# Optimization experiments

Measured on AMD Instinct MI355X. Metric: run time of the kernel, lower is better.

The kernel has to match this reference:

```python
import jax, jax.numpy as jnp
import numpy as np

D = 64          # hidden_dim
H = 4           # num_attention_heads
L = 3           # num_layers
NUM_SEG = 32    # graphs per batch
N_MOL, N_PROT = 4096, 8192
E_MOL, E_PROT = 65536, 262144
LN_EPS = 1e-5


def linear(x, w, b):
    return x @ w + b


def gine_conv(x, edge_index, edge_attr, w1, b1, w2, b2, num_nodes):
    # GINEConv (eps=0): nn(x_i + sum_{j->i} relu(x_j + e_ij))
    src, dst = edge_index[0], edge_index[1]
    msg = jax.nn.relu(x[src] + edge_attr)                      # [E, D]
    agg = jax.ops.segment_sum(msg, dst, num_segments=num_nodes)
    h = jax.nn.relu(linear(x + agg, w1, b1))
    return linear(h, w2, b2)


def cross_attn(q_nodes, k_nodes, qkv_w, qkv_b):
    # qkv_w: [3, D, D] stacked (Q, K, V)
    dh = D // H
    Q = (q_nodes @ qkv_w[0] + qkv_b[0]).reshape(-1, H, dh)
    K = (k_nodes @ qkv_w[1] + qkv_b[1]).reshape(-1, H, dh)
    V = (k_nodes @ qkv_w[2] + qkv_b[2]).reshape(-1, H, dh)
    scale = jnp.asarray(dh, Q.dtype) ** 0.5
    scores = jnp.einsum('qhd,khd->hqk', Q, K) / scale          # [H, Nq, Nk]
    attn = jax.nn.softmax(scores, axis=-1)
    out = jnp.einsum('hqk,khd->qhd', attn, V)                  # [Nq, H, dh]
    return out.reshape(q_nodes.shape[0], D)


def layer_norm(x, g, b):
    mu = x.mean(-1, keepdims=True)
    var = x.var(-1, keepdims=True)
    return (x - mu) / jnp.sqrt(var + LN_EPS) * g + b


def mean_pool(x, batch):
    s = jax.ops.segment_sum(x, batch, num_segments=NUM_SEG)
    c = jax.ops.segment_sum(jnp.ones((x.shape[0],), x.dtype), batch, num_segments=NUM_SEG)
    return s / jnp.maximum(c, 1.0)[:, None]


def setup_inputs() -> dict:
    key = jax.random.key(0)
    ks = iter(jax.random.split(key, 64))
    s = 0.05
    inp = {}
    inp['mol_x'] = jax.random.normal(next(ks), (N_MOL, 11), jnp.float32)
    inp['prot_x'] = jax.random.normal(next(ks), (N_PROT, 15), jnp.float32)
    inp['mol_edge_attr'] = jax.random.normal(next(ks), (E_MOL, 10), jnp.float32)
    inp['prot_edge_attr'] = jax.random.normal(next(ks), (E_PROT, 10), jnp.float32)
    inp['init_node_mol_w'] = jax.random.normal(next(ks), (11, D), jnp.float32) * s
    inp['init_node_mol_b'] = jnp.zeros((D,), jnp.float32)
    inp['init_node_prot_w'] = jax.random.normal(next(ks), (15, D), jnp.float32) * s
    inp['init_node_prot_b'] = jnp.zeros((D,), jnp.float32)
    inp['init_edge_mol_w'] = jax.random.normal(next(ks), (10, D), jnp.float32) * s
    inp['init_edge_mol_b'] = jnp.zeros((D,), jnp.float32)
    inp['init_edge_prot_w'] = jax.random.normal(next(ks), (10, D), jnp.float32) * s
    inp['init_edge_prot_b'] = jnp.zeros((D,), jnp.float32)
    for g in ['mol', 'prot']:
        inp[f'gine_{g}_w1'] = jax.random.normal(next(ks), (L, D, D), jnp.float32) * s
        inp[f'gine_{g}_b1'] = jnp.zeros((L, D), jnp.float32)
        inp[f'gine_{g}_w2'] = jax.random.normal(next(ks), (L, D, D), jnp.float32) * s
        inp[f'gine_{g}_b2'] = jnp.zeros((L, D), jnp.float32)
    inp['m2p_qkv_w'] = jax.random.normal(next(ks), (L, 3, D, D), jnp.float32) * s
    inp['m2p_qkv_b'] = jnp.zeros((L, 3, D), jnp.float32)
    inp['p2m_qkv_w'] = jax.random.normal(next(ks), (L, 3, D, D), jnp.float32) * s
    inp['p2m_qkv_b'] = jnp.zeros((L, 3, D), jnp.float32)
    inp['ln_mol_g'] = jnp.ones((L, D), jnp.float32)
    inp['ln_mol_b'] = jnp.zeros((L, D), jnp.float32)
    inp['ln_prot_g'] = jnp.ones((L, D), jnp.float32)
    inp['ln_prot_b'] = jnp.zeros((L, D), jnp.float32)
    inp['fc1_w'] = jax.random.normal(next(ks), (2 * D, D), jnp.float32) * s
    inp['fc1_b'] = jnp.zeros((D,), jnp.float32)
    inp['fc2_w'] = jax.random.normal(next(ks), (D, 1), jnp.float32) * s
    inp['fc2_b'] = jnp.zeros((1,), jnp.float32)
    inp['mol_edge_index'] = jax.random.randint(next(ks), (2, E_MOL), 0, N_MOL, jnp.int32)
    inp['prot_edge_index'] = jax.random.randint(next(ks), (2, E_PROT), 0, N_PROT, jnp.int32)
    inp['mol_batch'] = jnp.sort(jax.random.randint(next(ks), (N_MOL,), 0, NUM_SEG, jnp.int32))
    inp['prot_batch'] = jnp.sort(jax.random.randint(next(ks), (N_PROT,), 0, NUM_SEG, jnp.int32))
    return inp


def reference(mol_x, prot_x, mol_edge_attr, prot_edge_attr,
              init_node_mol_w, init_node_mol_b, init_node_prot_w, init_node_prot_b,
              init_edge_mol_w, init_edge_mol_b, init_edge_prot_w, init_edge_prot_b,
              gine_mol_w1, gine_mol_b1, gine_mol_w2, gine_mol_b2,
              gine_prot_w1, gine_prot_b1, gine_prot_w2, gine_prot_b2,
              m2p_qkv_w, m2p_qkv_b, p2m_qkv_w, p2m_qkv_b,
              ln_mol_g, ln_mol_b, ln_prot_g, ln_prot_b,
              fc1_w, fc1_b, fc2_w, fc2_b,
              mol_edge_index, prot_edge_index, mol_batch, prot_batch):
    x_mol = linear(mol_x, init_node_mol_w, init_node_mol_b)
    x_prot = linear(prot_x, init_node_prot_w, init_node_prot_b)
    ea_mol = linear(mol_edge_attr, init_edge_mol_w, init_edge_mol_b)
    ea_prot = linear(prot_edge_attr, init_edge_prot_w, init_edge_prot_b)
    n_mol, n_prot = x_mol.shape[0], x_prot.shape[0]
    for l in range(L):
        h_mol = jax.nn.relu(gine_conv(x_mol, mol_edge_index, ea_mol,
                                      gine_mol_w1[l], gine_mol_b1[l],
                                      gine_mol_w2[l], gine_mol_b2[l], n_mol))
        h_prot = jax.nn.relu(gine_conv(x_prot, prot_edge_index, ea_prot,
                                       gine_prot_w1[l], gine_prot_b1[l],
                                       gine_prot_w2[l], gine_prot_b2[l], n_prot))
        a_mol = cross_attn(h_mol, h_prot, m2p_qkv_w[l], m2p_qkv_b[l])
        a_prot = cross_attn(h_prot, h_mol, p2m_qkv_w[l], p2m_qkv_b[l])
        x_mol = layer_norm(h_mol + a_mol, ln_mol_g[l], ln_mol_b[l])
        x_prot = layer_norm(h_prot + a_prot, ln_prot_g[l], ln_prot_b[l])
    z = jnp.concatenate([mean_pool(x_mol, mol_batch), mean_pool(x_prot, prot_batch)], axis=1)
    h = jax.nn.relu(z @ fc1_w + fc1_b)
    out = jax.nn.sigmoid(h @ fc2_w + fc2_b)
    return out.squeeze(-1)   # [NUM_SEG]
```

## Files before the change

### kernel.cpp

```cpp
#include <hip/hip_runtime.h>
#include <cstddef>

typedef _Float16 f16x4 __attribute__((ext_vector_type(4)));
typedef __fp16 h16x2 __attribute__((ext_vector_type(2)));
typedef float f32x4 __attribute__((ext_vector_type(4)));

__device__ __forceinline__ f32x4 mfma16(f16x4 a, f16x4 b, f32x4 c) {
  return __builtin_amdgcn_mfma_f32_16x16x16f16(a, b, c, 0, 0, 0);
}

__device__ __forceinline__ float fast_exp2(float x) {
#if __has_builtin(__builtin_amdgcn_exp2f)
  return __builtin_amdgcn_exp2f(x);
#else
  return exp2f(x);
#endif
}

#define QSCALE (0.25f * 1.44269504f)
#define NSPLIT 8
#define NMC 4096
#define NPC 8192
#define EMC 65536
#define EPC 262144
#define NTOT (NMC + NPC)
#define ETOT (EMC + EPC)

__global__ __launch_bounds__(256) void init_embed_dual(
    const float* __restrict__ inm, const float* __restrict__ Wm,
    const float* __restrict__ bm, float* __restrict__ outm,
    const float* __restrict__ inp, const float* __restrict__ Wp,
    const float* __restrict__ bp, float* __restrict__ outp)
{
  int idx = blockIdx.x * 256 + threadIdx.x;
  const float *in, *W, *bb;
  float* out;
  int Kin;
  if (idx < NMC * 64) {
    in = inm; W = Wm; bb = bm; out = outm; Kin = 11;
  } else {
    idx -= NMC * 64;
    if (idx >= NPC * 64) return;
    in = inp; W = Wp; bb = bp; out = outp; Kin = 15;
  }
  int n = idx >> 6, o = idx & 63;
  float acc = bb[o];
  const float* row = in + (size_t)n * Kin;
  for (int k = 0; k < Kin; k++) acc += row[k] * W[k * 64 + o];
  out[idx] = acc;
}

__global__ __launch_bounds__(256) void deg_hist_kernel(
    const int* __restrict__ eim, const int* __restrict__ eip, int* __restrict__ deg)
{
  int idx = blockIdx.x * 256 + threadIdx.x;
  if (idx >= ETOT) return;
  int dst = (idx < EMC) ? eim[EMC + idx] : (eip[EPC + (idx - EMC)] + NMC);
  atomicAdd(&deg[dst], 1);
}

__global__ __launch_bounds__(1024) void scan_kernel(
    const int* __restrict__ deg, int* __restrict__ rowStart, int* __restrict__ cursor)
{
  __shared__ int part[1024];
  int t = threadIdx.x;
  int base = t * 12;
  int local[12];
  int s = 0;
  #pragma unroll
  for (int i = 0; i < 12; i++) { local[i] = s; s += deg[base + i]; }
  part[t] = s;
  __syncthreads();
  #pragma unroll
  for (int d = 1; d < 1024; d <<= 1) {
    int v = (t >= d) ? part[t - d] : 0;
    __syncthreads();
    part[t] += v;
    __syncthreads();
  }
  int prefix = (t == 0) ? 0 : part[t - 1];
  #pragma unroll
  for (int i = 0; i < 12; i++) {
    int v = prefix + local[i];
    rowStart[base + i] = v;
    cursor[base + i] = v;
  }
  if (t == 1023) rowStart[NTOT] = prefix + s;
}

__global__ __launch_bounds__(256) void fill_kernel(
    const int* __restrict__ eim, const int* __restrict__ eip,
    int* __restrict__ cursor, int* __restrict__ srcPerm, int* __restrict__ slotOf)
{
  int idx = blockIdx.x * 256 + threadIdx.x;
  if (idx >= ETOT) return;
  int src, dst;
  if (idx < EMC) {
    src = eim[idx]; dst = eim[EMC + idx];
  } else {
    int e = idx - EMC; src = eip[e]; dst = eip[EPC + e] + NMC;
  }
  int slot = atomicAdd(&cursor[dst], 1);
  srcPerm[slot] = src;
  slotOf[idx] = slot;
}

__global__ __launch_bounds__(256) void attr_perm_kernel(
    const int* __restrict__ slotOf,
    const float* __restrict__ attrm, const float* __restrict__ attrp,
    float* __restrict__ attrPerm)
{
  int idx = blockIdx.x * 256 + threadIdx.x;
  int e = idx >> 4, k = idx & 15;
  if (e >= ETOT || k >= 12) return;
  float v = 0.f;
  if (k < 10)
    v = (e < EMC) ? attrm[(size_t)e * 10 + k] : attrp[(size_t)(e - EMC) * 10 + k];
  attrPerm[(size_t)slotOf[e] * 12 + k] = v;
}

__global__ __launch_bounds__(256) void ea_lin_kernel(
    const float* __restrict__ attrPerm,
    const float* __restrict__ Wem, const float* __restrict__ bem,
    const float* __restrict__ Wep, const float* __restrict__ bep,
    _Float16* __restrict__ eaPerm)
{
  __shared__ __align__(16) float sAttr[128 * 12];
  __shared__ float sWe[10 * 64];
  __shared__ float sBe[64];
  int t = threadIdx.x;
  int s0 = blockIdx.x * 128;
  const float* We = (s0 < EMC) ? Wem : Wep;
  const float* be = (s0 < EMC) ? bem : bep;
  #pragma unroll
  for (int i = 0; i < 6; i++) {
    int f = t + i * 256;
    sAttr[f] = attrPerm[(size_t)s0 * 12 + f];
  }
  for (int f = t; f < 640; f += 256) sWe[f] = We[f];
  if (t < 64) sBe[t] = be[t];
  __syncthreads();
  int sl = t >> 1;
  int d0 = (t & 1) * 32;
  float at[10];
  #pragma unroll
  for (int k = 0; k < 10; k++) at[k] = sAttr[sl * 12 + k];
  _Float16 outv[32];
  #pragma unroll
  for (int j = 0; j < 32; j++) {
    int d = d0 + j;
    float ea = sBe[d];
    #pragma unroll
    for (int k = 0; k < 10; k++) ea += at[k] * sWe[k * 64 + d];
    outv[j] = (_Float16)ea;
  }
  float4* dst = (float4*)(eaPerm + (size_t)(s0 + sl) * 64 + d0);
  const float4* src = (const float4*)outv;
  #pragma unroll
  for (int j = 0; j < 4; j++) dst[j] = src[j];
}

__global__ __launch_bounds__(256) void gine_gather_kernel(
    const float* __restrict__ xm, const float* __restrict__ xp,
    const int* __restrict__ rowStart, const int* __restrict__ srcPerm,
    const _Float16* __restrict__ eaPerm,
    float* __restrict__ aggm, float* __restrict__ aggp)
{
  int n = (blockIdx.x * 256 + threadIdx.x) >> 6;
  int lane = threadIdx.x & 63;
  if (n >= NTOT) return;
  const float* x;
  float* agg;
  int nl;
  if (n < NMC) { x = xm; agg = aggm; nl = n; }
  else         { x = xp; agg = aggp; nl = n - NMC; }
  int b0 = rowStart[n], b1 = rowStart[n + 1];
  float acc = 0.f;
  int i = b0;
  for (; i + 3 < b1; i += 4) {
    int s0 = srcPerm[i], s1 = srcPerm[i + 1], s2 = srcPerm[i + 2], s3 = srcPerm[i + 3];
    float e0 = (float)eaPerm[(size_t)i * 64 + lane];
    float e1 = (float)eaPerm[(size_t)(i + 1) * 64 + lane];
    float e2 = (float)eaPerm[(size_t)(i + 2) * 64 + lane];
    float e3 = (float)eaPerm[(size_t)(i + 3) * 64 + lane];
    float x0 = x[(size_t)s0 * 64 + lane];
    float x1 = x[(size_t)s1 * 64 + lane];
    float x2 = x[(size_t)s2 * 64 + lane];
    float x3 = x[(size_t)s3 * 64 + lane];
    acc += fmaxf(x0 + e0, 0.f) + fmaxf(x1 + e1, 0.f)
         + fmaxf(x2 + e2, 0.f) + fmaxf(x3 + e3, 0.f);
  }
  for (; i < b1; i++) {
    int src = srcPerm[i];
    float m = x[(size_t)src * 64 + lane] + (float)eaPerm[(size_t)i * 64 + lane];
    acc += fmaxf(m, 0.f);
  }
  agg[(size_t)nl * 64 + lane] = acc;
}

__global__ __launch_bounds__(256) void mlp_proj_dual(
    const float* __restrict__ xm, const float* __restrict__ aggm,
    const float* __restrict__ W1m, const float* __restrict__ B1m,
    const float* __restrict__ W2m, const float* __restrict__ B2m,
    float* __restrict__ hm,
    const float* __restrict__ Wqm, const float* __restrict__ bqm,
    const float* __restrict__ Wkm, const float* __restrict__ bkm,
    const float* __restrict__ Wvm, const float* __restrict__ bvm,
    _Float16* __restrict__ Qom, _Float16* __restrict__ Kom, _Float16* __restrict__ Vtom,
    const float* __restrict__ xp, const float* __restrict__ aggp,
    const float* __restrict__ W1p, const float* __restrict__ B1p,
    const float* __restrict__ W2p, const float* __restrict__ B2p,
    float* __restrict__ hp,
    const float* __restrict__ Wqp, const float* __restrict__ bqp,
    const float* __restrict__ Wkp, const float* __restrict__ bkp,
    const float* __restrict__ Wvp, const float* __restrict__ bvp,
    _Float16* __restrict__ Qop, _Float16* __restrict__ Kop, _Float16* __restrict__ Vtop)
{
  __shared__ __align__(16) float sW[64 * 64];
  __shared__ __align__(16) float sBuf[64 * 68];
  int t = threadIdx.x;
  int b = blockIdx.x;
  const float *x, *agg, *W1, *B1, *W2, *B2, *Wq, *bq, *Wk, *bk, *Wv, *bv;
  float* hg;
  _Float16 *Qo, *Ko, *Vto;
  int n0, N;
  if (b < 64) {
    x = xm; agg = aggm; W1 = W1m; B1 = B1m; W2 = W2m; B2 = B2m; hg = hm;
    Wq = Wqm; bq = bqm; Wk = Wkm; bk = bkm; Wv = Wvm; bv = bvm;
    Qo = Qom; Ko = Kom; Vto = Vtom; n0 = b * 64; N = NMC;
  } else {
    x = xp; agg = aggp; W1 = W1p; B1 = B1p; W2 = W2p; B2 = B2p; hg = hp;
    Wq = Wqp; bq = bqp; Wk = Wkp; bk = bkp; Wv = Wvp; bv = bvp;
    Qo = Qop; Ko = Kop; Vto = Vtop; n0 = (b - 64) * 64; N = NPC;
  }
  int n = t >> 2, kk = t & 3;
  float acc[16];

  #pragma unroll
  for (int i = 0; i < 16; i++) {
    int f = t + i * 256;
    size_t g = (size_t)n0 * 64 + f;
    sBuf[(f >> 6) * 68 + (f & 63)] = x[g] + agg[g];
    sW[f] = W1[f];
  }
  __syncthreads();
  #pragma unroll
  for (int j = 0; j < 16; j++) acc[j] = B1[kk * 16 + j];
  #pragma unroll
  for (int d = 0; d < 64; d++) {
    float xv = sBuf[n * 68 + d];
    const float* wrow = &sW[d * 64 + kk * 16];
    #pragma unroll
    for (int j = 0; j < 16; j++) acc[j] += xv * wrow[j];
  }
  __syncthreads();
  #pragma unroll
  for (int j = 0; j < 16; j++) sBuf[n * 68 + kk * 16 + j] = fmaxf(acc[j], 0.f);
  #pragma unroll
  for (int i = 0; i < 16; i++) { int f = t + i * 256; sW[f] = W2[f]; }
  __syncthreads();
  #pragma unroll
  for (int j = 0; j < 16; j++) acc[j] = B2[kk * 16 + j];
  #pragma unroll
  for (int d = 0; d < 64; d++) {
    float xv = sBuf[n * 68 + d];
    const float* wrow = &sW[d * 64 + kk * 16];
    #pragma unroll
    for (int j = 0; j < 16; j++) acc[j] += xv * wrow[j];
  }
  float* hop = hg + (size_t)(n0 + n) * 64 + kk * 16;
  #pragma unroll
  for (int j = 0; j < 16; j++) {
    acc[j] = fmaxf(acc[j], 0.f);
    hop[j] = acc[j];
  }
  __syncthreads();
  #pragma unroll
  for (int j = 0; j < 16; j++) sBuf[n * 68 + kk * 16 + j] = acc[j];

  const float* Ws[3] = {Wq, Wk, Wv};
  const float* bs[3] = {bq, bk, bv};
  for (int p = 0; p < 3; p++) {
    if (p > 0) __syncthreads();
    #pragma unroll
    for (int i = 0; i < 16; i++) { int f = t + i * 256; sW[f] = Ws[p][f]; }
    __syncthreads();
    #pragma unroll
    for (int j = 0; j < 16; j++) acc[j] = bs[p][kk * 16 + j];
    #pragma unroll
    for (int d = 0; d < 64; d++) {
      float xv = sBuf[n * 68 + d];
      const float* wrow = &sW[d * 64 + kk * 16];
      #pragma unroll
      for (int j = 0; j < 16; j++) acc[j] += xv * wrow[j];
    }
    if (p == 2) {
      #pragma unroll
      for (int j = 0; j < 16; j++)
        Vto[((size_t)kk * 16 + j) * N + (n0 + n)] = (_Float16)acc[j];
    } else {
      float scale = (p == 0) ? QSCALE : 1.0f;
      _Float16 tmp[16];
      #pragma unroll
      for (int j = 0; j < 16; j++) tmp[j] = (_Float16)(acc[j] * scale);
      _Float16* base = (p == 0) ? Qo : Ko;
      float4* dst = (float4*)(base + ((size_t)kk * N + n0 + n) * 16);
      dst[0] = ((float4*)tmp)[0];
      dst[1] = ((float4*)tmp)[1];
    }
  }
}

__global__ __launch_bounds__(256, 4) void attn_split_kernel(
    const _Float16* __restrict__ Qm, const _Float16* __restrict__ Kp,
    const _Float16* __restrict__ Vtp, float* __restrict__ OPm, float* __restrict__ LPm,
    const _Float16* __restrict__ Qp, const _Float16* __restrict__ Km,
    const _Float16* __restrict__ Vtm, float* __restrict__ OPp, float* __restrict__ LPp)
{
  const int bx = blockIdx.x;
  const _Float16 *Q, *K, *Vt;
  float *Opart, *Lpart;
  int Nq, Nk, qb;
  if (bx < 32) { Q = Qm; K = Kp; Vt = Vtp; Opart = OPm; Lpart = LPm; Nq = NMC; Nk = NPC; qb = bx; }
  else         { Q = Qp; K = Km; Vt = Vtm; Opart = OPp; Lpart = LPp; Nq = NPC; Nk = NMC; qb = bx - 32; }
  const int h = blockIdx.y;
  const int split = blockIdx.z;
  const int Ks = Nk / NSPLIT;
  const int q0 = qb * 128;
  const int t = threadIdx.x;
  const int wave = t >> 6, lane = t & 63;
  const int l16 = lane & 15, quad = lane >> 4;

  f16x4 qf[8];
  #pragma unroll
  for (int g = 0; g < 8; g++)
    qf[g] = *(const f16x4*)(Q + ((size_t)h * Nq + q0 + g * 16 + l16) * 16 + quad * 4);
  const _Float16* Kh = K + (size_t)h * Nk * 16;
  const _Float16* Vh = Vt + ((size_t)h * 16 + l16) * Nk;

  f32x4 oacc[8];
  float lacc[8];
  #pragma unroll
  for (int g = 0; g < 8; g++) { oacc[g] = (f32x4){0.f,0.f,0.f,0.f}; lacc[g] = 0.f; }
  const f32x4 zero = {0.f, 0.f, 0.f, 0.f};
  const h16x2 ones2 = {(__fp16)1.f, (__fp16)1.f};

  union PF { f16x4 v4; h16x2 h2[2]; };

  auto process = [&](const f16x4* kf, const f16x4* vf) {
    #pragma unroll
    for (int g = 0; g < 8; g++) {
      f32x4 s[4];
      #pragma unroll
      for (int c = 0; c < 4; c++) s[c] = mfma16(kf[c], qf[g], zero);
      f16x4 pf[4];
      #pragma unroll
      for (int c = 0; c < 4; c++) {
        float p0 = fast_exp2(s[c][0]);
        float p1 = fast_exp2(s[c][1]);
        float p2 = fast_exp2(s[c][2]);
        float p3 = fast_exp2(s[c][3]);
        PF u;
        u.h2[0] = __builtin_amdgcn_cvt_pkrtz(p0, p1);
        u.h2[1] = __builtin_amdgcn_cvt_pkrtz(p2, p3);
        pf[c] = u.v4;
        lacc[g] = __builtin_amdgcn_fdot2(u.h2[0], ones2, lacc[g], false);
        lacc[g] = __builtin_amdgcn_fdot2(u.h2[1], ones2, lacc[g], false);
      }
      #pragma unroll
      for (int c = 0; c < 4; c++) oacc[g] = mfma16(vf[c], pf[c], oacc[g]);
    }
  };

  const int kend = (split + 1) * Ks;
  int kb = split * Ks + wave * 64;
  for (; kb + 256 < kend; kb += 512) {
    f16x4 kfA[4], vfA[4], kfB[4], vfB[4];
    #pragma unroll
    for (int c = 0; c < 4; c++) {
      kfA[c] = *(const f16x4*)(Kh + (size_t)(kb + c * 16 + l16) * 16 + quad * 4);
      vfA[c] = *(const f16x4*)(Vh + kb + c * 16 + quad * 4);
    }
    #pragma unroll
    for (int c = 0; c < 4; c++) {
      kfB[c] = *(const f16x4*)(Kh + (size_t)(kb + 256 + c * 16 + l16) * 16 + quad * 4);
      vfB[c] = *(const f16x4*)(Vh + kb + 256 + c * 16 + quad * 4);
    }
    process(kfA, vfA);
    process(kfB, vfB);
  }
  for (; kb < kend; kb += 256) {
    f16x4 kf[4], vf[4];
    #pragma unroll
    for (int c = 0; c < 4; c++) {
      kf[c] = *(const f16x4*)(Kh + (size_t)(kb + c * 16 + l16) * 16 + quad * 4);
      vf[c] = *(const f16x4*)(Vh + kb + c * 16 + quad * 4);
    }
    process(kf, vf);
  }

  #pragma unroll
  for (int g = 0; g < 8; g++) {
    lacc[g] += __shfl_xor(lacc[g], 16);
    lacc[g] += __shfl_xor(lacc[g], 32);
  }

  __shared__ float sO[4][4][16][17];
  __shared__ float sLw[8][4][16];
  if (quad == 0) {
    #pragma unroll
    for (int g = 0; g < 8; g++) sLw[g][wave][l16] = lacc[g];
  }
  int q = t >> 4, d = t & 15;
  #pragma unroll
  for (int pass = 0; pass < 2; pass++) {
    __syncthreads();
    #pragma unroll
    for (int gg = 0; gg < 4; gg++) {
      int g = pass * 4 + gg;
      #pragma unroll
      for (int r = 0; r < 4; r++) sO[gg][wave][quad * 4 + r][l16] = oacc[g][r];
    }
    __syncthreads();
    #pragma unroll
    for (int gg = 0; gg < 4; gg++) {
      int g = pass * 4 + gg;
      float O = 0.f;
      #pragma unroll
      for (int w = 0; w < 4; w++) O += sO[gg][w][d][q];
      size_t row = (size_t)split * Nq + q0 + g * 16 + q;
      Opart[row * 64 + h * 16 + d] = O;
      if (d == 0) {
        float L = sLw[g][0][q] + sLw[g][1][q] + sLw[g][2][q] + sLw[g][3][q];
        Lpart[row * 4 + h] = L;
      }
    }
  }
}

__global__ __launch_bounds__(256) void ln_combine_dual(
    const float* __restrict__ hm, const float* __restrict__ Om,
    const float* __restrict__ Lm, const float* __restrict__ gm,
    const float* __restrict__ bm, float* __restrict__ outm,
    const float* __restrict__ hp, const float* __restrict__ Op,
    const float* __restrict__ Lp, const float* __restrict__ gp,
    const float* __restrict__ bp, float* __restrict__ outp)
{
  int idx = blockIdx.x * 256 + threadIdx.x;
  const float *hb, *Opart, *Lpart, *g, *bb;
  float* out;
  int N;
  int totalM = NMC * 64;
  if (idx < totalM) {
    hb = hm; Opart = Om; Lpart = Lm; g = gm; bb = bm; out = outm; N = NMC;
  } else {
    idx -= totalM;
    if (idx >= NPC * 64) return;
    hb = hp; Opart = Op; Lpart = Lp; g = gp; bb = bp; out = outp; N = NPC;
  }
  int n = idx >> 6, d = idx & 63, h = d >> 4;
  float O = 0.f, L = 0.f;
  #pragma unroll
  for (int s = 0; s < NSPLIT; s++) {
    size_t row = (size_t)s * N + n;
    O += Opart[row * 64 + d];
    L += Lpart[row * 4 + h];
  }
  float v = hb[idx] + O / L;
  float sm = v;
  #pragma unroll
  for (int o = 1; o < 64; o <<= 1) sm += __shfl_xor(sm, o);
  float mu = sm * 0.015625f;
  float c = v - mu;
  float q = c * c;
  #pragma unroll
  for (int o = 1; o < 64; o <<= 1) q += __shfl_xor(q, o);
  float var = q * 0.015625f;
  out[idx] = c * rsqrtf(var + 1e-5f) * g[d] + bb[d];
}

__global__ __launch_bounds__(256) void pool_run_kernel(
    const float* __restrict__ xm, const int* __restrict__ bm,
    const float* __restrict__ xp, const int* __restrict__ bp,
    float* __restrict__ sums, float* __restrict__ cnt)
{
  int wid = (blockIdx.x * 256 + threadIdx.x) >> 6;
  int lane = threadIdx.x & 63;
  const float* x;
  const int* batch;
  int n0, colOff, cntOff;
  if (wid < 64) {
    x = xm; batch = bm; n0 = wid * 64; colOff = 0; cntOff = 0;
  } else {
    wid -= 64;
    if (wid >= 128) return;
    x = xp; batch = bp; n0 = wid * 64; colOff = 64; cntOff = 32;
  }
  float acc = 0.f;
  int cur = batch[n0];
  int run = 0;
  for (int i = 0; i < 64; i++) {
    int n = n0 + i;
    int s = batch[n];
    if (s != cur) {
      atomicAdd(&sums[cur * 128 + colOff + lane], acc);
      if (lane == 0) atomicAdd(&cnt[cntOff + cur], (float)run);
      acc = 0.f; run = 0; cur = s;
    }
    acc += x[(size_t)n * 64 + lane];
    run++;
  }
  atomicAdd(&sums[cur * 128 + colOff + lane], acc);
  if (lane == 0) atomicAdd(&cnt[cntOff + cur], (float)run);
}

__global__ __launch_bounds__(256) void final_kernel(
    const float* __restrict__ sums, const float* __restrict__ cnt,
    const float* __restrict__ fc1w, const float* __restrict__ fc1b,
    const float* __restrict__ fc2w, const float* __restrict__ fc2b,
    float* __restrict__ out)
{
  __shared__ float z[32 * 128];
  __shared__ float h1[32 * 64];
  int t = threadIdx.x;
  for (int f = t; f < 32 * 128; f += 256) {
    int s = f >> 7, j = f & 127;
    float c = cnt[(j >> 6) * 32 + s];
    z[f] = sums[f] / fmaxf(c, 1.f);
  }
  __syncthreads();
  for (int f = t; f < 32 * 64; f += 256) {
    int s = f >> 6, o = f & 63;
    float acc = fc1b[o];
    for (int j = 0; j < 128; j++) acc += z[s * 128 + j] * fc1w[j * 64 + o];
    h1[f] = fmaxf(acc, 0.f);
  }
  __syncthreads();
  if (t < 32) {
    float acc = fc2b[0];
    for (int o = 0; o < 64; o++) acc += h1[t * 64 + o] * fc2w[o];
    out[t] = 1.f / (1.f + __expf(-acc));
  }
}

extern "C" void kernel_launch(void* const* d_in, const int* in_sizes, int n_in,
                              void* d_out, int out_size, void* d_ws, size_t ws_size,
                              hipStream_t stream)
{
  (void)in_sizes; (void)n_in; (void)out_size; (void)ws_size;
  const float* mol_x          = (const float*)d_in[0];
  const float* prot_x         = (const float*)d_in[1];
  const float* mol_edge_attr  = (const float*)d_in[2];
  const float* prot_edge_attr = (const float*)d_in[3];
  const float* inm_w = (const float*)d_in[4];
  const float* inm_b = (const float*)d_in[5];
  const float* inp_w = (const float*)d_in[6];
  const float* inp_b = (const float*)d_in[7];
  const float* iem_w = (const float*)d_in[8];
  const float* iem_b = (const float*)d_in[9];
  const float* iep_w = (const float*)d_in[10];
  const float* iep_b = (const float*)d_in[11];
  const float* gm_w1 = (const float*)d_in[12];
  const float* gm_b1 = (const float*)d_in[13];
  const float* gm_w2 = (const float*)d_in[14];
  const float* gm_b2 = (const float*)d_in[15];
  const float* gp_w1 = (const float*)d_in[16];
  const float* gp_b1 = (const float*)d_in[17];
  const float* gp_w2 = (const float*)d_in[18];
  const float* gp_b2 = (const float*)d_in[19];
  const float* m2p_w = (const float*)d_in[20];
  const float* m2p_b = (const float*)d_in[21];
  const float* p2m_w = (const float*)d_in[22];
  const float* p2m_b = (const float*)d_in[23];
  const float* lnm_g = (const float*)d_in[24];
  const float* lnm_b = (const float*)d_in[25];
  const float* lnp_g = (const float*)d_in[26];
  const float* lnp_b = (const float*)d_in[27];
  const float* fc1_w = (const float*)d_in[28];
  const float* fc1_b = (const float*)d_in[29];
  const float* fc2_w = (const float*)d_in[30];
  const float* fc2_b = (const float*)d_in[31];
  const int* mol_ei     = (const int*)d_in[32];
  const int* prot_ei    = (const int*)d_in[33];
  const int* mol_batch  = (const int*)d_in[34];
  const int* prot_batch = (const int*)d_in[35];

  const int NM = NMC, NP = NPC;

  float* ws = (float*)d_ws;
  size_t off = 0;
  auto nxt  = [&](size_t n) { float* p = ws + off; off += n; return p; };
  auto nxtH = [&](size_t n) { _Float16* p = (_Float16*)(ws + off); off += (n + 1) / 2; return p; };
  auto nxtI = [&](size_t n) { int* p = (int*)(ws + off); off += n; return p; };
  float* x_mol    = nxt((size_t)NM * 64);
  float* x_prot   = nxt((size_t)NP * 64);
  float* agg_mol  = nxt((size_t)NM * 64);
  float* agg_prot = nxt((size_t)NP * 64);
  float* h_mol    = nxt((size_t)NM * 64);
  float* h_prot   = nxt((size_t)NP * 64);
  _Float16* Qm  = nxtH((size_t)NM * 64);
  _Float16* Km  = nxtH((size_t)NM * 64);
  _Float16* Vtm = nxtH((size_t)NM * 64);
  _Float16* Qp  = nxtH((size_t)NP * 64);
  _Float16* Kp  = nxtH((size_t)NP * 64);
  _Float16* Vtp = nxtH((size_t)NP * 64);
  float* OPm = nxt((size_t)NSPLIT * NM * 64);
  float* LPm = nxt((size_t)NSPLIT * NM * 4);
  float* OPp = nxt((size_t)NSPLIT * NP * 64);
  float* LPp = nxt((size_t)NSPLIT * NP * 4);
  float* pool = nxt(32 * 128);
  float* cnt  = nxt(64);
  int* deg      = nxtI(NTOT);
  int* rowStart = nxtI(NTOT + 1);
  int* cursor   = nxtI(NTOT);
  int* slotOf   = nxtI(ETOT);
  int* srcPerm  = nxtI(ETOT);
  float* attrPerm = nxt((size_t)ETOT * 12);
  _Float16* eaPerm = nxtH((size_t)ETOT * 64);

  (void)hipMemsetAsync(deg, 0, NTOT * 4, stream);
  deg_hist_kernel<<<(ETOT + 255) / 256, 256, 0, stream>>>(mol_ei, prot_ei, deg);
  scan_kernel<<<1, 1024, 0, stream>>>(deg, rowStart, cursor);
  fill_kernel<<<(ETOT + 255) / 256, 256, 0, stream>>>(mol_ei, prot_ei, cursor, srcPerm, slotOf);
  attr_perm_kernel<<<ETOT * 16 / 256, 256, 0, stream>>>(slotOf, mol_edge_attr,
                                                        prot_edge_attr, attrPerm);
  ea_lin_kernel<<<ETOT / 128, 256, 0, stream>>>(attrPerm, iem_w, iem_b, iep_w, iep_b, eaPerm);

  init_embed_dual<<<(NM + NP) * 64 / 256, 256, 0, stream>>>(
      mol_x, inm_w, inm_b, x_mol, prot_x, inp_w, inp_b, x_prot);

  for (int l = 0; l < 3; l++) {
    gine_gather_kernel<<<NTOT / 4, 256, 0, stream>>>(x_mol, x_prot, rowStart, srcPerm,
                                                     eaPerm, agg_mol, agg_prot);
    mlp_proj_dual<<<192, 256, 0, stream>>>(
        x_mol, agg_mol, gm_w1 + l * 4096, gm_b1 + l * 64, gm_w2 + l * 4096, gm_b2 + l * 64, h_mol,
        m2p_w + (l * 3 + 0) * 4096, m2p_b + (l * 3 + 0) * 64,
        p2m_w + (l * 3 + 1) * 4096, p2m_b + (l * 3 + 1) * 64,
        p2m_w + (l * 3 + 2) * 4096, p2m_b + (l * 3 + 2) * 64,
        Qm, Km, Vtm,
        x_prot, agg_prot, gp_w1 + l * 4096, gp_b1 + l * 64, gp_w2 + l * 4096, gp_b2 + l * 64, h_prot,
        p2m_w + (l * 3 + 0) * 4096, p2m_b + (l * 3 + 0) * 64,
        m2p_w + (l * 3 + 1) * 4096, m2p_b + (l * 3 + 1) * 64,
        m2p_w + (l * 3 + 2) * 4096, m2p_b + (l * 3 + 2) * 64,
        Qp, Kp, Vtp);
    attn_split_kernel<<<dim3(96, 4, NSPLIT), 256, 0, stream>>>(
        Qm, Kp, Vtp, OPm, LPm, Qp, Km, Vtm, OPp, LPp);
    ln_combine_dual<<<(NM + NP) * 64 / 256, 256, 0, stream>>>(
        h_mol, OPm, LPm, lnm_g + l * 64, lnm_b + l * 64, x_mol,
        h_prot, OPp, LPp, lnp_g + l * 64, lnp_b + l * 64, x_prot);
  }

  (void)hipMemsetAsync(pool, 0, (32 * 128 + 64) * 4, stream);
  pool_run_kernel<<<48, 256, 0, stream>>>(x_mol, mol_batch, x_prot, prot_batch, pool, cnt);
  final_kernel<<<1, 256, 0, stream>>>(pool, cnt, fc1_w, fc1_b, fc2_w, fc2_b, (float*)d_out);
}
```

Baseline: 591.4 us.

## Use MFMA fp16 for GINE MLP and QKV projections, halve attention splits

Rewrites the fused MLP+QKV projection kernel to stage activations and transposed weights in fp16 shared memory and compute all five 64x64 GEMMs with 16x16x16 MFMA instructions instead of scalar fp32 FMAs. Each wave now owns a 16-column output slice, and the V-transpose store is vectorized. It also lowers the attention key split count from 8 to 4, trading parallelism for less partial-result merging. The GINE MLP intermediates now run in fp16, which reduces precision.

```diff
diff --git a/kernel.cpp b/kernel.cpp
--- a/kernel.cpp
+++ b/kernel.cpp
@@ -18,7 +18,7 @@
 }
 
 #define QSCALE (0.25f * 1.44269504f)
-#define NSPLIT 8
+#define NSPLIT 4
 #define NMC 4096
 #define NPC 8192
 #define EMC 65536
@@ -216,8 +216,10 @@
     const float* __restrict__ Wvp, const float* __restrict__ bvp,
     _Float16* __restrict__ Qop, _Float16* __restrict__ Kop, _Float16* __restrict__ Vtop)
 {
-  __shared__ __align__(16) float sW[64 * 64];
-  __shared__ __align__(16) float sBuf[64 * 68];
+  __shared__ __align__(16) _Float16 sA[64 * 68];
+  __shared__ __align__(16) _Float16 sB[64 * 68];
+  __shared__ __align__(16) _Float16 sWt[64 * 68];
+  __shared__ float sBias[64];
   int t = threadIdx.x;
   int b = blockIdx.x;
   const float *x, *agg, *W1, *B1, *W2, *B2, *Wq, *bq, *Wk, *bk, *Wv, *bv;
@@ -233,80 +235,112 @@
     Wq = Wqp; bq = bqp; Wk = Wkp; bk = bkp; Wv = Wvp; bv = bvp;
     Qo = Qop; Ko = Kop; Vto = Vtop; n0 = (b - 64) * 64; N = NPC;
   }
-  int n = t >> 2, kk = t & 3;
-  float acc[16];
+  const int wave = t >> 6, lane = t & 63;
+  const int l16 = lane & 15, quad = lane >> 4;
+
+  auto stageW = [&](const float* W, const float* bias) {
+    #pragma unroll
+    for (int i = 0; i < 16; i++) {
+      int f = t + i * 256;
+      sWt[(f & 63) * 68 + (f >> 6)] = (_Float16)W[f];
+    }
+    if (t < 64) sBias[t] = bias[t];
+  };
+
+  f32x4 acc[4];
+  auto gemm = [&](const _Float16* src) {
+    #pragma unroll
+    for (int mt = 0; mt < 4; mt++) acc[mt] = (f32x4){0.f, 0.f, 0.f, 0.f};
+    #pragma unroll
+    for (int ks = 0; ks < 4; ks++) {
+      f16x4 bf = *(const f16x4*)(sWt + (wave * 16 + l16) * 68 + ks * 16 + quad * 4);
+      #pragma unroll
+      for (int mt = 0; mt < 4; mt++) {
+        f16x4 af = *(const f16x4*)(src + (mt * 16 + l16) * 68 + ks * 16 + quad * 4);
+        acc[mt] = mfma16(af, bf, acc[mt]);
+      }
+    }
+  };
 
   #pragma unroll
   for (int i = 0; i < 16; i++) {
     int f = t + i * 256;
     size_t g = (size_t)n0 * 64 + f;
-    sBuf[(f >> 6) * 68 + (f & 63)] = x[g] + agg[g];
-    sW[f] = W1[f];
-  }
+    sA[(f >> 6) * 68 + (f & 63)] = (_Float16)(x[g] + agg[g]);
+  }
+  stageW(W1, B1);
   __syncthreads();
-  #pragma unroll
-  for (int j = 0; j < 16; j++) acc[j] = B1[kk * 16 + j];
-  #pragma unroll
-  for (int d = 0; d < 64; d++) {
-    float xv = sBuf[n * 68 + d];
-    const float* wrow = &sW[d * 64 + kk * 16];
-    #pragma unroll
-    for (int j = 0; j < 16; j++) acc[j] += xv * wrow[j];
-  }
-  __syncthreads();
-  #pragma unroll
-  for (int j = 0; j < 16; j++) sBuf[n * 68 + kk * 16 + j] = fmaxf(acc[j], 0.f);
-  #pragma unroll
-  for (int i = 0; i < 16; i++) { int f = t + i * 256; sW[f] = W2[f]; }
-  __syncthreads();
-  #pragma unroll
-  for (int j = 0; j < 16; j++) acc[j] = B2[kk * 16 + j];
-  #pragma unroll
-  for (int d = 0; d < 64; d++) {
-    float xv = sBuf[n * 68 + d];
-    const float* wrow = &sW[d * 64 + kk * 16];
-    #pragma unroll
-    for (int j = 0; j < 16; j++) acc[j] += xv * wrow[j];
-  }
-  float* hop = hg + (size_t)(n0 + n) * 64 + kk * 16;
-  #pragma unroll
-  for (int j = 0; j < 16; j++) {
-    acc[j] = fmaxf(acc[j], 0.f);
-    hop[j] = acc[j];
-  }
-  __syncthreads();
-  #pragma unroll
-  for (int j = 0; j < 16; j++) sBuf[n * 68 + kk * 16 + j] = acc[j];
-
-  const float* Ws[3] = {Wq, Wk, Wv};
-  const float* bs[3] = {bq, bk, bv};
-  for (int p = 0; p < 3; p++) {
-    if (p > 0) __syncthreads();
-    #pragma unroll
-    for (int i = 0; i < 16; i++) { int f = t + i * 256; sW[f] = Ws[p][f]; }
-    __syncthreads();
-    #pragma unroll
-    for (int j = 0; j < 16; j++) acc[j] = bs[p][kk * 16 + j];
-    #pragma unroll
-    for (int d = 0; d < 64; d++) {
-      float xv = sBuf[n * 68 + d];
-      const float* wrow = &sW[d * 64 + kk * 16];
-      #pragma unroll
-      for (int j = 0; j < 16; j++) acc[j] += xv * wrow[j];
-    }
-    if (p == 2) {
-      #pragma unroll
-      for (int j = 0; j < 16; j++)
-        Vto[((size_t)kk * 16 + j) * N + (n0 + n)] = (_Float16)acc[j];
-    } else {
-      float scale = (p == 0) ? QSCALE : 1.0f;
-      _Float16 tmp[16];
-      #pragma unroll
-      for (int j = 0; j < 16; j++) tmp[j] = (_Float16)(acc[j] * scale);
-      _Float16* base = (p == 0) ? Qo : Ko;
-      float4* dst = (float4*)(base + ((size_t)kk * N + n0 + n) * 16);
-      dst[0] = ((float4*)tmp)[0];
-      dst[1] = ((float4*)tmp)[1];
+
+  int od = wave * 16 + l16;
+
+  {
+    float bias = sBias[od];
+    gemm(sA);
+    __syncthreads();
+    #pragma unroll
+    for (int mt = 0; mt < 4; mt++)
+      #pragma unroll
+      for (int r = 0; r < 4; r++) {
+        int node = mt * 16 + quad * 4 + r;
+        sB[node * 68 + od] = (_Float16)fmaxf(acc[mt][r] + bias, 0.f);
+      }
+    stageW(W2, B2);
+    __syncthreads();
+  }
+  {
+    float bias = sBias[od];
+    gemm(sB);
+    __syncthreads();
+    #pragma unroll
+    for (int mt = 0; mt < 4; mt++)
+      #pragma unroll
+      for (int r = 0; r < 4; r++) {
+        int node = mt * 16 + quad * 4 + r;
+        float v = fmaxf(acc[mt][r] + bias, 0.f);
+        hg[(size_t)(n0 + node) * 64 + od] = v;
+        sA[node * 68 + od] = (_Float16)v;
+      }
+    stageW(Wq, bq);
+    __syncthreads();
+  }
+  {
+    float bias = sBias[od];
+    gemm(sA);
+    __syncthreads();
+    #pragma unroll
+    for (int mt = 0; mt < 4; mt++)
+      #pragma unroll
+      for (int r = 0; r < 4; r++) {
+        int node = mt * 16 + quad * 4 + r;
+        Qo[((size_t)wave * N + n0 + node) * 16 + l16] =
+            (_Float16)((acc[mt][r] + bias) * QSCALE);
+      }
+    stageW(Wk, bk);
+    __syncthreads();
+  }
+  {
+    float bias = sBias[od];
+    gemm(sA);
+    __syncthreads();
+    #pragma unroll
+    for (int mt = 0; mt < 4; mt++)
+      #pragma unroll
+      for (int r = 0; r < 4; r++) {
+        int node = mt * 16 + quad * 4 + r;
+        Ko[((size_t)wave * N + n0 + node) * 16 + l16] = (_Float16)(acc[mt][r] + bias);
+      }
+    stageW(Wv, bv);
+    __syncthreads();
+  }
+  {
+    float bias = sBias[od];
+    gemm(sA);
+    #pragma unroll
+    for (int mt = 0; mt < 4; mt++) {
+      f16x4 pk;
+      #pragma unroll
+      for (int r = 0; r < 4; r++) pk[r] = (_Float16)(acc[mt][r] + bias);
+      *(f16x4*)(Vto + ((size_t)wave * 16 + l16) * N + n0 + mt * 16 + quad * 4) = pk;
     }
   }
 }
```

Measured after the change: 506.2 us. 1.17x faster.
